# Optimization experiments

Hardware: AMD Instinct MI355X
Metric: run time of the kernel (lower is better)

## Reference

```python
import jax, jax.numpy as jnp
import numpy as np

N_NODES = 50000
N_EDGES = 600000
D = 128
THETA = (0.5, -1.0, 0.5)  # len(theta) must be 3 to match learnable_diag[3, in_feats]


def setup_inputs() -> dict:
    key = jax.random.key(0)
    k1, k2, k3, k4, k5 = jax.random.split(key, 5)
    feat = jax.random.normal(k1, (N_NODES, D), dtype=jnp.float32)
    edge_index = jax.random.randint(k2, (2, N_EDGES), 0, N_NODES)  # [src; dst]
    # learnable_diag = torch.rand(3, in_feats)
    diag = jax.random.uniform(k3, (3, D), dtype=jnp.float32)
    # nn.Linear(out_feats, out_feats) with xavier_uniform weight, zero bias
    limit = float(np.sqrt(6.0 / (D + D)))
    W = jax.random.uniform(k4, (D, D), dtype=jnp.float32, minval=-limit, maxval=limit)
    b = jnp.zeros((D,), dtype=jnp.float32)
    return {"feat": feat, "edge_index": edge_index, "diag": diag, "W": W, "b": b}


def reference(feat, edge_index, diag, W, b):
    src, dst = edge_index[0], edge_index[1]
    n = feat.shape[0]
    # in_degrees: count of incoming edges per node
    deg = jax.ops.segment_sum(jnp.ones_like(dst, dtype=feat.dtype), dst, num_segments=n)
    d_invsqrt = jnp.clip(deg, 1.0, None) ** -0.5  # [N]
    d_invsqrt = d_invsqrt[:, None]  # [N,1]

    h = (THETA[0] * feat) * diag[0]
    h = h @ W.T + b  # nn.Linear

    for k in range(1, len(THETA)):
        # unnLaplacian: feat - (A @ (feat * Dinv)) * Dinv * diag[k]
        msg = feat * d_invsqrt  # [N,D]
        agg = jax.ops.segment_sum(msg[src], dst, num_segments=n)  # SpMM: copy_u + sum
        feat = feat - agg * d_invsqrt * diag[k]
        h = h + THETA[k] * feat
    return h
```

## Files before the change

### kernel.cpp

```cpp
#include <hip/hip_runtime.h>

#define NN 50000
#define NE 600000
#define D  128
#define NBLK 196

typedef __attribute__((ext_vector_type(8))) short bf16x8;
typedef __attribute__((ext_vector_type(4))) float floatx4;

__device__ __forceinline__ unsigned short bf16_rne(float f) {
    union { float f; unsigned u; } v; v.f = f;
    unsigned r = v.u + 0x7FFFu + ((v.u >> 16) & 1u);
    return (unsigned short)(r >> 16);
}
__device__ __forceinline__ unsigned pack2(float a, float b) {
    return (unsigned)bf16_rne(a) | ((unsigned)bf16_rne(b) << 16);
}

__global__ __launch_bounds__(256) void prep_kernel(const float* __restrict__ W,
                                                   const float* __restrict__ diag,
                                                   unsigned short* __restrict__ Wb,
                                                   int* __restrict__ deg_i,
                                                   unsigned int* __restrict__ zrow0,
                                                   unsigned int* __restrict__ zrow1) {
    int g = blockIdx.x * 256 + threadIdx.x;
    if (g < NN) deg_i[g] = 0;
    if (g < 16384) {
        int j = g & 127;
        Wb[g] = bf16_rne(0.5f * diag[j] * W[g]);
    }
    if (g < 64) { zrow0[g] = 0u; zrow1[g] = 0u; }
}

__global__ __launch_bounds__(256) void hist_kernel(const int* __restrict__ dst,
                                                   int* __restrict__ deg_i) {
    int e = blockIdx.x * 256 + threadIdx.x;
    if (e < NE) atomicAdd(&deg_i[dst[e]], 1);
}

__global__ __launch_bounds__(256) void scan1_kernel(const int* __restrict__ deg_i,
                                                    int* __restrict__ row_ptr,
                                                    int* __restrict__ partials,
                                                    float* __restrict__ dinvf,
                                                    float* __restrict__ rdegf) {
    __shared__ int sh[256];
    int i = blockIdx.x * 256 + threadIdx.x;
    int dg = (i < NN) ? deg_i[i] : 0;
    if (i < NN) {
        float d = (float)dg;
        float dc = d > 1.0f ? d : 1.0f;
        dinvf[i] = rsqrtf(dc);
        rdegf[i] = sqrtf(dc);
    }
    sh[threadIdx.x] = dg;
    __syncthreads();
    #pragma unroll
    for (int off = 1; off < 256; off <<= 1) {
        int t = (threadIdx.x >= off) ? sh[threadIdx.x - off] : 0;
        __syncthreads();
        sh[threadIdx.x] += t;
        __syncthreads();
    }
    if (i < NN) row_ptr[i + 1] = sh[threadIdx.x];
    if (threadIdx.x == 255) partials[blockIdx.x] = sh[255];
}

__global__ __launch_bounds__(256) void scan23_kernel(int* __restrict__ row_ptr,
                                                     const int* __restrict__ partials,
                                                     int* __restrict__ fillc) {
    __shared__ int sh[256];
    const int t = threadIdx.x;
    sh[t] = (t < NBLK) ? partials[t] : 0;
    __syncthreads();
    #pragma unroll
    for (int off = 1; off < 256; off <<= 1) {
        int v = (t >= off) ? sh[t - off] : 0;
        __syncthreads();
        sh[t] += v;
        __syncthreads();
    }
    const int add = (blockIdx.x > 0) ? sh[blockIdx.x - 1] : 0;
    const int i = blockIdx.x * 256 + t;
    if (i < NN) {
        row_ptr[i + 1] += add;
        fillc[i] = 0;
    }
    if (i == 0) row_ptr[0] = 0;
}

__global__ __launch_bounds__(256) void fill_kernel(const int* __restrict__ src,
                                                   const int* __restrict__ dst,
                                                   const int* __restrict__ row_ptr,
                                                   int* __restrict__ fillc,
                                                   int* __restrict__ csr) {
    int e = blockIdx.x * 256 + threadIdx.x;
    if (e < NE) {
        int t = dst[e];
        int pos = row_ptr[t] + atomicAdd(&fillc[t], 1);
        csr[pos] = src[e];
    }
}

__global__ __launch_bounds__(256) void gemm_mfma_kernel(const float* __restrict__ feat,
                                                        const unsigned short* __restrict__ Wb,
                                                        const float* __restrict__ b,
                                                        const float* __restrict__ dinvf,
                                                        unsigned short* __restrict__ featb_s,
                                                        float* __restrict__ out) {
    const int wv   = threadIdx.x >> 6;
    const int lane = threadIdx.x & 63;
    const int r16  = lane & 15;
    const int quad = lane >> 4;
    const int m0   = blockIdx.x * 64 + wv * 16;

    const int mrow = m0 + r16;
    const int mc   = (mrow < NN) ? mrow : (NN - 1);
    const float* arow = feat + (size_t)mc * D + quad * 8;
    const float di = dinvf[mc];

    bf16x8 afrag[4];
    #pragma unroll
    for (int kc = 0; kc < 4; ++kc) {
        const float4 f0 = *(const float4*)(arow + kc * 32);
        const float4 f1 = *(const float4*)(arow + kc * 32 + 4);
        bf16x8 a;
        a[0] = (short)bf16_rne(f0.x); a[1] = (short)bf16_rne(f0.y);
        a[2] = (short)bf16_rne(f0.z); a[3] = (short)bf16_rne(f0.w);
        a[4] = (short)bf16_rne(f1.x); a[5] = (short)bf16_rne(f1.y);
        a[6] = (short)bf16_rne(f1.z); a[7] = (short)bf16_rne(f1.w);
        afrag[kc] = a;
        if (mrow < NN) {
            uint4 st;
            st.x = pack2(f0.x * di, f0.y * di);
            st.y = pack2(f0.z * di, f0.w * di);
            st.z = pack2(f1.x * di, f1.y * di);
            st.w = pack2(f1.z * di, f1.w * di);
            *(uint4*)(featb_s + (size_t)mc * D + quad * 8 + kc * 32) = st;
        }
    }

    floatx4 acc[8];
    #pragma unroll
    for (int nt = 0; nt < 8; ++nt) acc[nt] = (floatx4)(0.0f);

    #pragma unroll
    for (int nt = 0; nt < 8; ++nt) {
        const unsigned short* brow = Wb + (size_t)(nt * 16 + r16) * D + quad * 8;
        #pragma unroll
        for (int kc = 0; kc < 4; ++kc) {
            const bf16x8 bfrag = *(const bf16x8*)(brow + kc * 32);
            acc[nt] = __builtin_amdgcn_mfma_f32_16x16x32_bf16(afrag[kc], bfrag, acc[nt], 0, 0, 0);
        }
    }

    #pragma unroll
    for (int nt = 0; nt < 8; ++nt) {
        const int d = nt * 16 + r16;
        const float bd = b[d];
        #pragma unroll
        for (int r = 0; r < 4; ++r) {
            const int i = m0 + quad * 4 + r;
            if (i < NN) out[(size_t)i * D + d] = acc[nt][r] + bd;
        }
    }
}

__device__ __forceinline__ float2 gather_acc(const unsigned short* __restrict__ rows,
                                             const int* __restrict__ csr,
                                             int e0, int e1, int lane) {
    float2 acc = make_float2(0.0f, 0.0f);
    for (int bse = e0; bse < e1; bse += 64) {
        int idx = bse + lane;
        int s = (idx < e1) ? csr[idx] : NN;
        int cnt8 = (min(64, e1 - bse) + 7) & ~7;
        for (int k = 0; k < cnt8; k += 8) {
            #pragma unroll
            for (int u = 0; u < 8; ++u) {
                int ss = __shfl(s, k + u);
                unsigned pv = *(const unsigned*)(rows + (size_t)ss * D + 2 * lane);
                acc.x += __uint_as_float(pv << 16);
                acc.y += __uint_as_float(pv & 0xFFFF0000u);
            }
        }
    }
    return acc;
}

__global__ __launch_bounds__(256) void gather1_kernel(const unsigned short* __restrict__ featb_s,
                                                      const int* __restrict__ csr,
                                                      const int* __restrict__ row_ptr,
                                                      const float* __restrict__ dinvf,
                                                      const float* __restrict__ diag,
                                                      const float* __restrict__ feat0,
                                                      unsigned int* __restrict__ feat1s) {
    const int node = blockIdx.x * 4 + (threadIdx.x >> 6);
    const int lane = threadIdx.x & 63;
    float2 acc = gather_acc(featb_s, csr, row_ptr[node], row_ptr[node + 1], lane);

    const size_t o2 = (size_t)node * (D / 2) + lane;
    const float di = dinvf[node];
    const float2 bs = *(const float2*)&feat0[2 * o2];
    const float2 dg = *(const float2*)&diag[D + 2 * lane];
    float rx = bs.x - acc.x * di * dg.x;
    float ry = bs.y - acc.y * di * dg.y;
    feat1s[o2] = pack2(rx * di, ry * di);
}

__global__ __launch_bounds__(256) void gather2_kernel(const unsigned short* __restrict__ feat1s,
                                                      const int* __restrict__ csr,
                                                      const int* __restrict__ row_ptr,
                                                      const float* __restrict__ dinvf,
                                                      const float* __restrict__ rdegf,
                                                      const float* __restrict__ diag,
                                                      float* __restrict__ outp) {
    const int node = blockIdx.x * 4 + (threadIdx.x >> 6);
    const int lane = threadIdx.x & 63;
    float2 acc = gather_acc(feat1s, csr, row_ptr[node], row_ptr[node + 1], lane);

    const size_t o2 = (size_t)node * (D / 2) + lane;
    const float di = dinvf[node];
    const float rd = rdegf[node];
    const unsigned bp = ((const unsigned*)feat1s)[o2];
    const float2 dg = *(const float2*)&diag[2 * D + 2 * lane];
    float bx = __uint_as_float(bp << 16) * rd;
    float by = __uint_as_float(bp & 0xFFFF0000u) * rd;
    float2 cur = *(const float2*)&outp[2 * o2];
    cur.x -= 0.5f * (bx + acc.x * di * dg.x);
    cur.y -= 0.5f * (by + acc.y * di * dg.y);
    *(float2*)&outp[2 * o2] = cur;
}

extern "C" void kernel_launch(void* const* d_in, const int* in_sizes, int n_in,
                              void* d_out, int out_size, void* d_ws, size_t ws_size,
                              hipStream_t stream) {
    const float* feat = (const float*)d_in[0];
    const int*   eidx = (const int*)d_in[1];
    const float* diag = (const float*)d_in[2];
    const float* W    = (const float*)d_in[3];
    const float* b    = (const float*)d_in[4];
    float* out = (float*)d_out;

    const int* src = eidx;
    const int* dst = eidx + NE;

    unsigned short* featb_s = (unsigned short*)d_ws;
    unsigned short* feat1s  = featb_s + (size_t)(NN + 1) * D;
    int*   csr      = (int*)(feat1s + (size_t)(NN + 1) * D);
    float* dinvf    = (float*)(csr + NE);
    float* rdegf    = dinvf + NN;
    int*   deg_i    = (int*)(rdegf + NN);
    int*   row_ptr  = deg_i + NN;
    int*   fillc    = row_ptr + NN + 2;
    int*   partials = fillc + NN;
    unsigned short* Wb = (unsigned short*)(partials + 256);

    prep_kernel<<<NBLK, 256, 0, stream>>>(W, diag, Wb, deg_i,
                                          (unsigned int*)(featb_s + (size_t)NN * D),
                                          (unsigned int*)(feat1s + (size_t)NN * D));

    hist_kernel<<<(NE + 255) / 256, 256, 0, stream>>>(dst, deg_i);
    scan1_kernel<<<NBLK, 256, 0, stream>>>(deg_i, row_ptr, partials, dinvf, rdegf);
    scan23_kernel<<<NBLK, 256, 0, stream>>>(row_ptr, partials, fillc);
    fill_kernel<<<(NE + 255) / 256, 256, 0, stream>>>(src, dst, row_ptr, fillc, csr);

    gemm_mfma_kernel<<<(NN + 63) / 64, 256, 0, stream>>>(feat, Wb, b, dinvf, featb_s, out);

    gather1_kernel<<<NN / 4, 256, 0, stream>>>(featb_s, csr, row_ptr, dinvf, diag,
                                               feat, (unsigned int*)feat1s);
    gather2_kernel<<<NN / 4, 256, 0, stream>>>(feat1s, csr, row_ptr, dinvf, rdegf, diag, out);
}
```

Before: 227.3 us.

## Gather two neighbor rows per wavefront with 8-byte loads; reuse degree counters for CSR fill

The SpMM gather now splits each 64-lane wavefront into two halves. Each half loads a different neighbor row with 8-byte loads, covering 4 bf16 features per lane, and the halves are combined at the end with a cross-half shuffle. This halves the number of shuffle and load instructions per edge and widens each memory access. Separately, the CSR fill decrements the existing degree counters instead of zeroing and incrementing a separate fill counter, which removes one array and its initialisation. The epilogue now runs only on half the lanes, which idles the other half during the writeback.

```diff
diff --git a/kernel.cpp b/kernel.cpp
--- a/kernel.cpp
+++ b/kernel.cpp
@@ -7,6 +7,7 @@
 
 typedef __attribute__((ext_vector_type(8))) short bf16x8;
 typedef __attribute__((ext_vector_type(4))) float floatx4;
+typedef __attribute__((ext_vector_type(2))) float f32x2;
 
 __device__ __forceinline__ unsigned short bf16_rne(float f) {
     union { float f; unsigned u; } v; v.f = f;
@@ -66,8 +67,7 @@
 }
 
 __global__ __launch_bounds__(256) void scan23_kernel(int* __restrict__ row_ptr,
-                                                     const int* __restrict__ partials,
-                                                     int* __restrict__ fillc) {
+                                                     const int* __restrict__ partials) {
     __shared__ int sh[256];
     const int t = threadIdx.x;
     sh[t] = (t < NBLK) ? partials[t] : 0;
@@ -81,23 +81,20 @@
     }
     const int add = (blockIdx.x > 0) ? sh[blockIdx.x - 1] : 0;
     const int i = blockIdx.x * 256 + t;
-    if (i < NN) {
-        row_ptr[i + 1] += add;
-        fillc[i] = 0;
-    }
+    if (i < NN) row_ptr[i + 1] += add;
     if (i == 0) row_ptr[0] = 0;
 }
 
 __global__ __launch_bounds__(256) void fill_kernel(const int* __restrict__ src,
                                                    const int* __restrict__ dst,
                                                    const int* __restrict__ row_ptr,
-                                                   int* __restrict__ fillc,
+                                                   int* __restrict__ deg_i,
                                                    int* __restrict__ csr) {
     int e = blockIdx.x * 256 + threadIdx.x;
     if (e < NE) {
         int t = dst[e];
-        int pos = row_ptr[t] + atomicAdd(&fillc[t], 1);
-        csr[pos] = src[e];
+        int c = atomicAdd(&deg_i[t], -1);
+        csr[row_ptr[t] + c - 1] = src[e];
     }
 }
 
@@ -165,25 +162,38 @@
     }
 }
 
-__device__ __forceinline__ float2 gather_acc(const unsigned short* __restrict__ rows,
-                                             const int* __restrict__ csr,
-                                             int e0, int e1, int lane) {
-    float2 acc = make_float2(0.0f, 0.0f);
+__device__ __forceinline__ floatx4 gather_acc(const unsigned short* __restrict__ rows,
+                                              const int* __restrict__ csr,
+                                              int e0, int e1, int lane) {
+    const int half = lane >> 5;
+    const unsigned lane_b = (unsigned)((lane & 31) << 3);
+    f32x2 a01 = (f32x2)(0.0f);
+    f32x2 a23 = (f32x2)(0.0f);
     for (int bse = e0; bse < e1; bse += 64) {
         int idx = bse + lane;
         int s = (idx < e1) ? csr[idx] : NN;
         int cnt8 = (min(64, e1 - bse) + 7) & ~7;
         for (int k = 0; k < cnt8; k += 8) {
             #pragma unroll
-            for (int u = 0; u < 8; ++u) {
-                int ss = __shfl(s, k + u);
-                unsigned pv = *(const unsigned*)(rows + (size_t)ss * D + 2 * lane);
-                acc.x += __uint_as_float(pv << 16);
-                acc.y += __uint_as_float(pv & 0xFFFF0000u);
+            for (int u = 0; u < 4; ++u) {
+                int ss = __shfl(s, k + 2 * u + half);
+                const uint2 pv = *(const uint2*)((const char*)rows +
+                                    (((unsigned)ss << 8) | lane_b));
+                f32x2 lo0, lo1;
+                lo0.x = __uint_as_float(pv.x << 16);
+                lo0.y = __uint_as_float(pv.x & 0xFFFF0000u);
+                lo1.x = __uint_as_float(pv.y << 16);
+                lo1.y = __uint_as_float(pv.y & 0xFFFF0000u);
+                a01 += lo0;
+                a23 += lo1;
             }
         }
     }
-    return acc;
+    floatx4 r;
+    r[0] = a01.x; r[1] = a01.y; r[2] = a23.x; r[3] = a23.y;
+    #pragma unroll
+    for (int i = 0; i < 4; ++i) r[i] += __shfl_xor(r[i], 32);
+    return r;
 }
 
 __global__ __launch_bounds__(256) void gather1_kernel(const unsigned short* __restrict__ featb_s,
@@ -192,18 +202,22 @@
                                                       const float* __restrict__ dinvf,
                                                       const float* __restrict__ diag,
                                                       const float* __restrict__ feat0,
-                                                      unsigned int* __restrict__ feat1s) {
+                                                      unsigned short* __restrict__ feat1s) {
     const int node = blockIdx.x * 4 + (threadIdx.x >> 6);
     const int lane = threadIdx.x & 63;
-    float2 acc = gather_acc(featb_s, csr, row_ptr[node], row_ptr[node + 1], lane);
-
-    const size_t o2 = (size_t)node * (D / 2) + lane;
-    const float di = dinvf[node];
-    const float2 bs = *(const float2*)&feat0[2 * o2];
-    const float2 dg = *(const float2*)&diag[D + 2 * lane];
-    float rx = bs.x - acc.x * di * dg.x;
-    float ry = bs.y - acc.y * di * dg.y;
-    feat1s[o2] = pack2(rx * di, ry * di);
+    floatx4 acc = gather_acc(featb_s, csr, row_ptr[node], row_ptr[node + 1], lane);
+    if (lane < 32) {
+        const int c0 = lane << 2;
+        const float di = dinvf[node];
+        const float4 bs = *(const float4*)(feat0 + (size_t)node * D + c0);
+        const float4 dg = *(const float4*)(diag + D + c0);
+        const float r0 = (bs.x - acc[0] * di * dg.x) * di;
+        const float r1 = (bs.y - acc[1] * di * dg.y) * di;
+        const float r2 = (bs.z - acc[2] * di * dg.z) * di;
+        const float r3 = (bs.w - acc[3] * di * dg.w) * di;
+        uint2 st; st.x = pack2(r0, r1); st.y = pack2(r2, r3);
+        *(uint2*)((char*)feat1s + ((size_t)node << 8) + (lane << 3)) = st;
+    }
 }
 
 __global__ __launch_bounds__(256) void gather2_kernel(const unsigned short* __restrict__ feat1s,
@@ -215,19 +229,24 @@
                                                       float* __restrict__ outp) {
     const int node = blockIdx.x * 4 + (threadIdx.x >> 6);
     const int lane = threadIdx.x & 63;
-    float2 acc = gather_acc(feat1s, csr, row_ptr[node], row_ptr[node + 1], lane);
-
-    const size_t o2 = (size_t)node * (D / 2) + lane;
-    const float di = dinvf[node];
-    const float rd = rdegf[node];
-    const unsigned bp = ((const unsigned*)feat1s)[o2];
-    const float2 dg = *(const float2*)&diag[2 * D + 2 * lane];
-    float bx = __uint_as_float(bp << 16) * rd;
-    float by = __uint_as_float(bp & 0xFFFF0000u) * rd;
-    float2 cur = *(const float2*)&outp[2 * o2];
-    cur.x -= 0.5f * (bx + acc.x * di * dg.x);
-    cur.y -= 0.5f * (by + acc.y * di * dg.y);
-    *(float2*)&outp[2 * o2] = cur;
+    floatx4 acc = gather_acc(feat1s, csr, row_ptr[node], row_ptr[node + 1], lane);
+    if (lane < 32) {
+        const int c0 = lane << 2;
+        const float di = dinvf[node];
+        const float rd = rdegf[node];
+        const uint2 bp = *(const uint2*)((const char*)feat1s + ((size_t)node << 8) + (lane << 3));
+        const float b0 = __uint_as_float(bp.x << 16) * rd;
+        const float b1 = __uint_as_float(bp.x & 0xFFFF0000u) * rd;
+        const float b2 = __uint_as_float(bp.y << 16) * rd;
+        const float b3 = __uint_as_float(bp.y & 0xFFFF0000u) * rd;
+        const float4 dg = *(const float4*)(diag + 2 * D + c0);
+        float4 cur = *(float4*)(outp + (size_t)node * D + c0);
+        cur.x -= 0.5f * (b0 + acc[0] * di * dg.x);
+        cur.y -= 0.5f * (b1 + acc[1] * di * dg.y);
+        cur.z -= 0.5f * (b2 + acc[2] * di * dg.z);
+        cur.w -= 0.5f * (b3 + acc[3] * di * dg.w);
+        *(float4*)(outp + (size_t)node * D + c0) = cur;
+    }
 }
 
 extern "C" void kernel_launch(void* const* d_in, const int* in_sizes, int n_in,
@@ -250,8 +269,7 @@
     float* rdegf    = dinvf + NN;
     int*   deg_i    = (int*)(rdegf + NN);
     int*   row_ptr  = deg_i + NN;
-    int*   fillc    = row_ptr + NN + 2;
-    int*   partials = fillc + NN;
+    int*   partials = row_ptr + NN + 2;
     unsigned short* Wb = (unsigned short*)(partials + 256);
 
     prep_kernel<<<NBLK, 256, 0, stream>>>(W, diag, Wb, deg_i,
@@ -260,12 +278,12 @@
 
     hist_kernel<<<(NE + 255) / 256, 256, 0, stream>>>(dst, deg_i);
     scan1_kernel<<<NBLK, 256, 0, stream>>>(deg_i, row_ptr, partials, dinvf, rdegf);
-    scan23_kernel<<<NBLK, 256, 0, stream>>>(row_ptr, partials, fillc);
-    fill_kernel<<<(NE + 255) / 256, 256, 0, stream>>>(src, dst, row_ptr, fillc, csr);
+    scan23_kernel<<<NBLK, 256, 0, stream>>>(row_ptr, partials);
+    fill_kernel<<<(NE + 255) / 256, 256, 0, stream>>>(src, dst, row_ptr, deg_i, csr);
 
     gemm_mfma_kernel<<<(NN + 63) / 64, 256, 0, stream>>>(feat, Wb, b, dinvf, featb_s, out);
 
     gather1_kernel<<<NN / 4, 256, 0, stream>>>(featb_s, csr, row_ptr, dinvf, diag,
-                                               feat, (unsigned int*)feat1s);
+                                               feat, feat1s);
     gather2_kernel<<<NN / 4, 256, 0, stream>>>(feat1s, csr, row_ptr, dinvf, rdegf, diag, out);
 }
```

After: 222.4 us. 1.02x faster.
